# Optimization experiments

Hardware: AMD Instinct MI355X
Metric: run time of the kernel (lower is better)

The kernel has to match this reference:

```python
import jax, jax.numpy as jnp
import numpy as np

N_NODES = 100000
NEG_SLOPE = 0.2


def _gat_conv(x, edge_index, W, att_src, att_dst, bias):
    """Single-head PyG-style GATConv with self-loops.
    x: [N, F_in], edge_index: [2, E] (row 0 = src j, row 1 = dst i).
    """
    N = x.shape[0]
    h = x @ W  # [N, F_out]
    # add self-loops
    loop = jnp.arange(N, dtype=edge_index.dtype)
    src = jnp.concatenate([edge_index[0], loop])
    dst = jnp.concatenate([edge_index[1], loop])
    # per-node attention terms, gathered per edge
    a_s = h @ att_src  # [N]
    a_d = h @ att_dst  # [N]
    e = jax.nn.leaky_relu(a_s[src] + a_d[dst], NEG_SLOPE)  # [E+N]
    # segment softmax over incoming edges of each destination
    m = jax.ops.segment_max(e, dst, num_segments=N)  # [N]
    m = jnp.where(jnp.isfinite(m), m, 0.0)
    p = jnp.exp(e - m[dst])
    denom = jax.ops.segment_sum(p, dst, num_segments=N)  # [N], >0 due to self-loops
    alpha = p / denom[dst]  # [E+N]
    # scatter-aggregate weighted source features
    out = jax.ops.segment_sum(h[src] * alpha[:, None], dst, num_segments=N)
    return out + bias


def setup_inputs() -> dict:
    key = jax.random.key(0)
    ks = jax.random.split(key, 12)
    F_in, H, C = 128, 64, 40
    x = jax.random.normal(ks[0], (N_NODES, F_in), dtype=jnp.float32)
    edge_index = jax.random.randint(ks[1], (2, 1600000), 0, N_NODES, dtype=jnp.int64)
    s1 = 1.0 / np.sqrt(F_in)
    s2 = 1.0 / np.sqrt(H)
    return {
        "x": x,
        "edge_index": edge_index,
        "W1": jax.random.uniform(ks[2], (F_in, H), jnp.float32, -s1, s1),
        "att_src1": jax.random.uniform(ks[3], (H,), jnp.float32, -s2, s2),
        "att_dst1": jax.random.uniform(ks[4], (H,), jnp.float32, -s2, s2),
        "b1": jnp.zeros((H,), jnp.float32),
        "W2": jax.random.uniform(ks[5], (H, C), jnp.float32, -s2, s2),
        "att_src2": jax.random.uniform(ks[6], (C,), jnp.float32, -1.0 / np.sqrt(C), 1.0 / np.sqrt(C)),
        "att_dst2": jax.random.uniform(ks[7], (C,), jnp.float32, -1.0 / np.sqrt(C), 1.0 / np.sqrt(C)),
        "b2": jnp.zeros((C,), jnp.float32),
    }


def reference(x, edge_index, W1, att_src1, att_dst1, b1, W2, att_src2, att_dst2, b2):
    h = _gat_conv(x, edge_index, W1, att_src1, att_dst1, b1)
    h = jax.nn.relu(h)
    # dropout is identity in eval mode
    out = _gat_conv(h, edge_index, W2, att_src2, att_dst2, b2)
    return out
```

## Files before the change

### kernel.cpp

```cpp
#include <hip/hip_runtime.h>
#include <math.h>


#define NEG_SLOPE 0.2f
#define BIN_SHIFT 8
#define BIN_NODES 256
#define MAXBINS   512
#define CAPB      4864
#define K1_CHUNK  4096
#define MAXDEG    128
#define AGG_STRIDE 132
#define XS1 136

typedef _Float16 h4_t __attribute__((ext_vector_type(4)));
typedef _Float16 h8_t __attribute__((ext_vector_type(8)));
typedef float    f16x_t __attribute__((ext_vector_type(16)));

__device__ __forceinline__ float lrelu(float v) {
    return v > 0.f ? v : NEG_SLOPE * v;
}

__global__ __launch_bounds__(256) void prep_kernel(
    const float* __restrict__ W1, const float* __restrict__ W2,
    const float* __restrict__ as1, const float* __restrict__ ad1,
    const float* __restrict__ as2, const float* __restrict__ ad2,
    _Float16* __restrict__ w1f, _Float16* __restrict__ w2f,
    float* __restrict__ u1, float* __restrict__ v1,
    int* __restrict__ bin_cursor)
{
    const int tid = threadIdx.x;
    if (blockIdx.x == 0) {
        for (int j = tid; j < MAXBINS; j += 256) bin_cursor[j] = 0;
        for (int i = tid; i < 8192; i += 256) {
            int j = i & 7, l = (i >> 3) & 63, q = i >> 9;
            int kc = q & 7, ch = q >> 3;
            int n = ch * 32 + (l & 31);
            int k = (l >> 5) * 8 + kc * 16 + j;
            w1f[i] = (_Float16)W1[k * 64 + n];
        }
        if (tid < 128) {
            float su = 0.f, sv = 0.f;
            for (int n = 0; n < 64; ++n) {
                float w = W1[tid * 64 + n];
                su += w * as1[n];
                sv += w * ad1[n];
            }
            u1[tid] = su; v1[tid] = sv;
        }
    } else {
        __shared__ float u2l[64], v2l[64];
        if (tid < 64) {
            float su = 0.f, sv = 0.f;
            for (int n = 0; n < 40; ++n) {
                float w = W2[tid * 40 + n];
                su += w * as2[n];
                sv += w * ad2[n];
            }
            u2l[tid] = su; v2l[tid] = sv;
        }
        __syncthreads();
        for (int i = tid; i < 4096; i += 256) {
            int j = i & 7, l = (i >> 3) & 63, q = i >> 9;
            int kc = q & 3, ch = q >> 2;
            int n = ch * 32 + (l & 31);
            int k = (l >> 5) * 8 + kc * 16 + j;
            _Float16 o = (_Float16)0.f;
            if (n < 40)       o = (_Float16)W2[k * 40 + n];
            else if (n == 40) o = (_Float16)u2l[k];
            else if (n == 41) o = (_Float16)v2l[k];
            w2f[i] = o;
        }
    }
}

__global__ __launch_bounds__(256) void gemm1_bin_kernel(
    const float* __restrict__ x, const _Float16* __restrict__ w1f,
    const float* __restrict__ u1, const float* __restrict__ v1,
    _Float16* __restrict__ h, float* __restrict__ as_, float* __restrict__ ad_,
    int N, int gb,
    const int* __restrict__ src, const int* __restrict__ dst, int E, int nbins,
    int* __restrict__ bin_cursor, int* __restrict__ binned)
{
    __shared__ __align__(16) char smem[18432];
    const int tid = threadIdx.x;

    if (blockIdx.x < gb) {
        _Float16* Xs = (_Float16*)smem;
        float*    Us = (float*)(smem + 17408);
        float*    Vs = (float*)(smem + 17920);
        const int lane = tid & 63;
        const int w = tid >> 6;
        const int rh = w >> 1, ch = w & 1;
        const long rowbase = (long)blockIdx.x * 64;

        {
            const float4* X4 = (const float4*)x;
            const long gmax = (long)N * 32;
#pragma unroll
            for (int i = 0; i < 8; ++i) {
                int f = tid + i * 256;
                int row = f >> 5, c4 = f & 31;
                long gi = (rowbase + row) * 32 + c4;
                float4 v = (gi < gmax) ? X4[gi] : make_float4(0.f, 0.f, 0.f, 0.f);
                h4_t hv;
                hv.x = (_Float16)v.x; hv.y = (_Float16)v.y;
                hv.z = (_Float16)v.z; hv.w = (_Float16)v.w;
                *(h4_t*)&Xs[row * XS1 + c4 * 4] = hv;
            }
        }
        if (tid < 128) Us[tid] = u1[tid];
        else { int t = tid - 128; Vs[t] = v1[t]; }
        __syncthreads();

        {
            const int arow = tid >> 2, apart = tid & 3;
            const _Float16* xr = &Xs[arow * XS1 + apart * 32];
            float ps = 0.f, pd = 0.f;
#pragma unroll
            for (int k = 0; k < 32; k += 4) {
                h4_t xv = *(const h4_t*)(xr + k);
                float4 uu = *(const float4*)&Us[apart * 32 + k];
                float4 vv = *(const float4*)&Vs[apart * 32 + k];
                float x0 = (float)xv.x, x1 = (float)xv.y, x2 = (float)xv.z, x3 = (float)xv.w;
                ps += x0 * uu.x + x1 * uu.y + x2 * uu.z + x3 * uu.w;
                pd += x0 * vv.x + x1 * vv.y + x2 * vv.z + x3 * vv.w;
            }
            ps += __shfl_xor(ps, 1); ps += __shfl_xor(ps, 2);
            pd += __shfl_xor(pd, 1); pd += __shfl_xor(pd, 2);
            if (apart == 0 && rowbase + arow < N) {
                as_[rowbase + arow] = ps;
                ad_[rowbase + arow] = pd;
            }
        }

        const int m = lane & 31, khalf = lane >> 5;
        const _Float16* ax = &Xs[(rh * 32 + m) * XS1 + khalf * 8];
        const h8_t* bF = (const h8_t*)w1f + ch * 8 * 64 + lane;

        f16x_t acc = {};
#pragma unroll
        for (int kc = 0; kc < 8; ++kc) {
            h8_t a = *(const h8_t*)(ax + kc * 16);
            h8_t b = bF[kc * 64];
            acc = __builtin_amdgcn_mfma_f32_32x32x16_f16(a, b, acc, 0, 0, 0);
        }

        const int col = ch * 32 + m;
#pragma unroll
        for (int r = 0; r < 16; ++r) {
            int rowl = (r & 3) + 8 * (r >> 2) + 4 * khalf;
            long grow = rowbase + rh * 32 + rowl;
            if (grow < N) h[grow * 64 + col] = (_Float16)acc[r];
        }
    } else {
        int* hist = (int*)smem;
        int* base = (int*)(smem + 2048);
        int* lcur = (int*)(smem + 4096);
        const int e0 = (blockIdx.x - gb) * K1_CHUNK;

        int sreg[16], dreg[16];
#pragma unroll
        for (int k = 0; k < 16; ++k) {
            int e = e0 + tid + k * 256;
            bool ok = e < E;
            dreg[k] = ok ? dst[e] : -1;
            sreg[k] = ok ? src[e] : 0;
        }

        for (int j = tid; j < nbins; j += 256) hist[j] = 0;
        __syncthreads();
#pragma unroll
        for (int k = 0; k < 16; ++k)
            if (dreg[k] >= 0) atomicAdd(&hist[dreg[k] >> BIN_SHIFT], 1);
        __syncthreads();
        for (int j = tid; j < nbins; j += 256) {
            int c = hist[j];
            base[j] = (c > 0) ? atomicAdd(&bin_cursor[j], c) : 0;
            lcur[j] = 0;
        }
        __syncthreads();
#pragma unroll
        for (int k = 0; k < 16; ++k) {
            if (dreg[k] >= 0) {
                int b = dreg[k] >> BIN_SHIFT;
                int o = atomicAdd(&lcur[b], 1);
                int pos = base[b] + o;
                if (pos < CAPB)
                    binned[b * CAPB + pos] =
                        (sreg[k] << BIN_SHIFT) | (dreg[k] & (BIN_NODES - 1));
            }
        }
    }
}

__global__ __launch_bounds__(512) void fine_kernel(
    const int* __restrict__ bin_cursor, const int* __restrict__ binned,
    int* __restrict__ csr, int* __restrict__ rowptr, int N, int nbins)
{
    __shared__ int a[MAXBINS];
    __shared__ int nh[BIN_NODES];
    __shared__ int cur[BIN_NODES];
    __shared__ int lbuf[CAPB];
    __shared__ int sb[2];
    const int b = blockIdx.x;
    const int tid = threadIdx.x;

    int v = (tid < nbins) ? min(bin_cursor[tid], CAPB) : 0;
    a[tid] = v;
    __syncthreads();
#pragma unroll
    for (int ofs = 1; ofs < MAXBINS; ofs <<= 1) {
        int t = (tid >= ofs) ? a[tid - ofs] : 0;
        __syncthreads();
        a[tid] += t;
        __syncthreads();
    }
    if (tid == 0) {
        sb[0] = (b > 0) ? a[b - 1] : 0;
        sb[1] = a[nbins - 1];
    }

    const int cnt = min(bin_cursor[b], CAPB);
    const int nn = min(BIN_NODES, N - b * BIN_NODES);
    const int* __restrict__ brec = binned + (long)b * CAPB;

    if (tid < BIN_NODES) nh[tid] = 0;
    __syncthreads();

    for (int k = tid; k < cnt; k += 512) {
        atomicAdd(&nh[brec[k] & (BIN_NODES - 1)], 1);
    }
    __syncthreads();

    int hv = (tid < BIN_NODES) ? nh[tid] : 0;
#pragma unroll
    for (int ofs = 1; ofs < BIN_NODES; ofs <<= 1) {
        int t = (tid >= ofs && tid < BIN_NODES) ? nh[tid - ofs] : 0;
        __syncthreads();
        if (tid < BIN_NODES) nh[tid] += t;
        __syncthreads();
    }
    const int binbase = sb[0];
    if (tid < BIN_NODES) {
        int excl = nh[tid] - hv;
        if (tid < nn) rowptr[b * BIN_NODES + tid] = binbase + excl;
        cur[tid] = excl;
    }
    if (b == nbins - 1 && tid == 0) rowptr[N] = sb[1];
    __syncthreads();

    for (int k = tid; k < cnt; k += 512) {
        int rec = brec[k];
        int pos = atomicAdd(&cur[rec & (BIN_NODES - 1)], 1);
        lbuf[pos] = rec >> BIN_SHIFT;
    }
    __syncthreads();
    for (int t = tid; t < cnt; t += 512) {
        csr[binbase + t] = lbuf[t];
    }
}

#define XS2 72
__global__ __launch_bounds__(256) void gemm2_kernel(
    const _Float16* __restrict__ hin, const _Float16* __restrict__ w2f,
    _Float16* __restrict__ h2, float* __restrict__ as_, float* __restrict__ ad_,
    int N)
{
    __shared__ __align__(16) _Float16 Xs[64 * XS2];
    const int tid = threadIdx.x;
    const int lane = tid & 63;
    const int w = tid >> 6;
    const int rh = w >> 1, ch = w & 1;
    const long rowbase = (long)blockIdx.x * 64;

    {
        const h8_t* X8 = (const h8_t*)hin;
        const long gmax = (long)N * 8;
#pragma unroll
        for (int i = 0; i < 2; ++i) {
            int f = tid + i * 256;
            int row = f >> 3, c = f & 7;
            long gi = (rowbase + row) * 8 + c;
            h8_t v = {};
            if (gi < gmax) v = X8[gi];
#pragma unroll
            for (int j = 0; j < 8; ++j) v[j] = (v[j] > (_Float16)0.f) ? v[j] : (_Float16)0.f;
            *(h8_t*)&Xs[row * XS2 + c * 8] = v;
        }
    }
    __syncthreads();

    const int m = lane & 31, khalf = lane >> 5;
    const _Float16* ax = &Xs[(rh * 32 + m) * XS2 + khalf * 8];
    const h8_t* bF = (const h8_t*)w2f + ch * 4 * 64 + lane;

    f16x_t acc = {};
#pragma unroll
    for (int kc = 0; kc < 4; ++kc) {
        h8_t a = *(const h8_t*)(ax + kc * 16);
        h8_t b = bF[kc * 64];
        acc = __builtin_amdgcn_mfma_f32_32x32x16_f16(a, b, acc, 0, 0, 0);
    }

    const int col = ch * 32 + m;
#pragma unroll
    for (int r = 0; r < 16; ++r) {
        int rowl = (r & 3) + 8 * (r >> 2) + 4 * khalf;
        long grow = rowbase + rh * 32 + rowl;
        float v = acc[r];
        if (grow < N) {
            if (col < 40)       h2[grow * 40 + col] = (_Float16)v;
            else if (col == 40) as_[grow] = v;
            else if (col == 41) ad_[grow] = v;
        }
    }
}

template<int F, typename OT>
__global__ __launch_bounds__(256) void aggregate_kernel(
    const _Float16* __restrict__ h, const float* __restrict__ as_,
    const float* __restrict__ ad_, const int* __restrict__ rowptr,
    const int* __restrict__ csr, const float* __restrict__ bias,
    OT* __restrict__ out, int N)
{
    __shared__ __align__(16) int   Ss[16 * AGG_STRIDE];
    __shared__ __align__(16) float Ps[16 * AGG_STRIDE];
    const int tid = threadIdx.x;
    const int dl  = tid >> 4;
    const int sub = tid & 15;
    const int i = blockIdx.x * 16 + dl;
    const bool alive = (i < N);

    int r0 = 0, deg = 0;
    if (alive) {
        r0 = rowptr[i];
        deg = rowptr[i + 1] - r0;
        if (deg > MAXDEG) deg = MAXDEG;
    }
    const float adi    = alive ? ad_[i] : 0.f;
    const float e_self = alive ? lrelu(as_[i] + adi) : 0.f;

    int*   __restrict__ sp = &Ss[dl * AGG_STRIDE];
    float* __restrict__ pp = &Ps[dl * AGG_STRIDE];

    float psum = 0.f;
    for (int c = sub; c < deg; c += 16) {
        int s = csr[r0 + c];
        float p = __expf(lrelu(as_[s] + adi));
        sp[c] = s;
        pp[c] = p;
        psum += p;
    }
#pragma unroll
    for (int off = 1; off < 16; off <<= 1) psum += __shfl_xor(psum, off);
    const float p_self = __expf(e_self);
    const float inv = 1.f / (psum + p_self);

    const bool act = (sub * 4 < F);
    const int  col = act ? sub * 4 : 0;
    float4 acc = make_float4(0.f, 0.f, 0.f, 0.f);

    int k = 0;
    for (; k + 8 <= deg; k += 8) {
        int4   s0 = *(const int4*)&sp[k];
        int4   s1 = *(const int4*)&sp[k + 4];
        float4 p0 = *(const float4*)&pp[k];
        float4 p1 = *(const float4*)&pp[k + 4];
        if (act) {
            h4_t hA = *(const h4_t*)&h[(long)s0.x * F + col];
            h4_t hB = *(const h4_t*)&h[(long)s0.y * F + col];
            h4_t hC = *(const h4_t*)&h[(long)s0.z * F + col];
            h4_t hD = *(const h4_t*)&h[(long)s0.w * F + col];
            h4_t hE = *(const h4_t*)&h[(long)s1.x * F + col];
            h4_t hF = *(const h4_t*)&h[(long)s1.y * F + col];
            h4_t hG = *(const h4_t*)&h[(long)s1.z * F + col];
            h4_t hH = *(const h4_t*)&h[(long)s1.w * F + col];
            acc.x += (float)hA.x * p0.x + (float)hB.x * p0.y + (float)hC.x * p0.z + (float)hD.x * p0.w
                   + (float)hE.x * p1.x + (float)hF.x * p1.y + (float)hG.x * p1.z + (float)hH.x * p1.w;
            acc.y += (float)hA.y * p0.x + (float)hB.y * p0.y + (float)hC.y * p0.z + (float)hD.y * p0.w
                   + (float)hE.y * p1.x + (float)hF.y * p1.y + (float)hG.y * p1.z + (float)hH.y * p1.w;
            acc.z += (float)hA.z * p0.x + (float)hB.z * p0.y + (float)hC.z * p0.z + (float)hD.z * p0.w
                   + (float)hE.z * p1.x + (float)hF.z * p1.y + (float)hG.z * p1.z + (float)hH.z * p1.w;
            acc.w += (float)hA.w * p0.x + (float)hB.w * p0.y + (float)hC.w * p0.z + (float)hD.w * p0.w
                   + (float)hE.w * p1.x + (float)hF.w * p1.y + (float)hG.w * p1.z + (float)hH.w * p1.w;
        }
    }
    for (; k + 4 <= deg; k += 4) {
        int4   s0 = *(const int4*)&sp[k];
        float4 p0 = *(const float4*)&pp[k];
        if (act) {
            h4_t hA = *(const h4_t*)&h[(long)s0.x * F + col];
            h4_t hB = *(const h4_t*)&h[(long)s0.y * F + col];
            h4_t hC = *(const h4_t*)&h[(long)s0.z * F + col];
            h4_t hD = *(const h4_t*)&h[(long)s0.w * F + col];
            acc.x += (float)hA.x * p0.x + (float)hB.x * p0.y + (float)hC.x * p0.z + (float)hD.x * p0.w;
            acc.y += (float)hA.y * p0.x + (float)hB.y * p0.y + (float)hC.y * p0.z + (float)hD.y * p0.w;
            acc.z += (float)hA.z * p0.x + (float)hB.z * p0.y + (float)hC.z * p0.z + (float)hD.z * p0.w;
            acc.w += (float)hA.w * p0.x + (float)hB.w * p0.y + (float)hC.w * p0.z + (float)hD.w * p0.w;
        }
    }
    for (; k < deg; ++k) {
        int   s = sp[k];
        float p = pp[k];
        if (act) {
            h4_t hv = *(const h4_t*)&h[(long)s * F + col];
            acc.x += (float)hv.x * p; acc.y += (float)hv.y * p;
            acc.z += (float)hv.z * p; acc.w += (float)hv.w * p;
        }
    }

    if (alive && act) {
        h4_t hv = *(const h4_t*)&h[(long)i * F + col];
        float4 bv = *(const float4*)&bias[col];
        float ox = (acc.x + (float)hv.x * p_self) * inv + bv.x;
        float oy = (acc.y + (float)hv.y * p_self) * inv + bv.y;
        float oz = (acc.z + (float)hv.z * p_self) * inv + bv.z;
        float ow = (acc.w + (float)hv.w * p_self) * inv + bv.w;
        if constexpr (sizeof(OT) == 4) {
            float4 o = make_float4(ox, oy, oz, ow);
            *(float4*)&out[(long)i * F + col] = o;
        } else {
            h4_t o;
            o.x = (_Float16)ox; o.y = (_Float16)oy;
            o.z = (_Float16)oz; o.w = (_Float16)ow;
            *(h4_t*)&out[(long)i * F + col] = o;
        }
    }
}

extern "C" void kernel_launch(void* const* d_in, const int* in_sizes, int n_in,
                              void* d_out, int out_size, void* d_ws, size_t ws_size,
                              hipStream_t stream) {
    const float* x    = (const float*)d_in[0];
    const int*   ei   = (const int*)d_in[1];
    const float* W1   = (const float*)d_in[2];
    const float* at_s1= (const float*)d_in[3];
    const float* at_d1= (const float*)d_in[4];
    const float* b1   = (const float*)d_in[5];
    const float* W2   = (const float*)d_in[6];
    const float* at_s2= (const float*)d_in[7];
    const float* at_d2= (const float*)d_in[8];
    const float* b2   = (const float*)d_in[9];
    float* out = (float*)d_out;

    const int N = in_sizes[0] / 128;
    const int E = in_sizes[1] / 2;
    const int nbins = (N + BIN_NODES - 1) >> BIN_SHIFT;

    char* p = (char*)d_ws;
    auto carve = [&](size_t bytes) -> void* {
        void* r = (void*)p;
        p += (bytes + 255) & ~(size_t)255;
        return r;
    };
    int*       bin_cursor = (int*)      carve((size_t)MAXBINS * 4);
    int*       binned     = (int*)      carve((size_t)nbins * CAPB * 4);
    int*       csr        = (int*)      carve((size_t)E * 4);
    int*       rowptr     = (int*)      carve((size_t)(N + 1) * 4);
    _Float16*  w1f        = (_Float16*) carve((size_t)8192 * 2);
    _Float16*  w2f        = (_Float16*) carve((size_t)4096 * 2);
    float*     u1         = (float*)    carve((size_t)128 * 4);
    float*     v1         = (float*)    carve((size_t)128 * 4);
    _Float16*  h1         = (_Float16*) carve((size_t)N * 64 * 2);
    _Float16*  agg1h      = (_Float16*) carve((size_t)N * 64 * 2);
    _Float16*  h2         = (_Float16*) carve((size_t)N * 40 * 2);
    float*     asn        = (float*)    carve((size_t)N * 4);
    float*     adn        = (float*)    carve((size_t)N * 4);

    prep_kernel<<<2, 256, 0, stream>>>(W1, W2, at_s1, at_d1, at_s2, at_d2,
                                       w1f, w2f, u1, v1, bin_cursor);

    const int gb = (N + 63) / 64;
    const int bb = (E + K1_CHUNK - 1) / K1_CHUNK;
    gemm1_bin_kernel<<<gb + bb, 256, 0, stream>>>(
        x, w1f, u1, v1, h1, asn, adn, N, gb,
        ei, ei + E, E, nbins, bin_cursor, binned);

    fine_kernel<<<nbins, 512, 0, stream>>>(bin_cursor, binned, csr, rowptr, N, nbins);

    aggregate_kernel<64, _Float16><<<(N + 15) / 16, 256, 0, stream>>>(
        h1, asn, adn, rowptr, csr, b1, agg1h, N);

    gemm2_kernel<<<(N + 63) / 64, 256, 0, stream>>>(agg1h, w2f, h2, asn, adn, N);

    aggregate_kernel<40, float><<<(N + 15) / 16, 256, 0, stream>>>(
        h2, asn, adn, rowptr, csr, b2, out, N);
}
```

Measured before the change: 222.9 us.

## Fuse layer-1 aggregation with layer-2 GEMM via per-block MFMA epilogue

Replaces the separate layer-1 aggregate kernel and gemm2 kernel with one kernel. Each 16-node block aggregates its neighbours, applies bias and ReLU, stages the fp16 rows in shared memory, and runs 16x16x32 MFMAs against a repacked W2 (with the attention vectors folded in) to emit h2 and the layer-2 attention scalars. This removes a kernel launch and the write and re-read of the intermediate N x 64 activation. In exchange each block does a small GEMM with only three of its four waves busy, adds a __syncthreads, and uses separate buffers for the layer-2 attention scalars.

Result: faster. 218.3 us (-2.1%).

```diff
diff --git a/kernel.cpp b/kernel.cpp
--- a/kernel.cpp
+++ b/kernel.cpp
@@ -11,10 +11,12 @@
 #define MAXDEG    128
 #define AGG_STRIDE 132
 #define XS1 136
+#define RTS 72
 
 typedef _Float16 h4_t __attribute__((ext_vector_type(4)));
 typedef _Float16 h8_t __attribute__((ext_vector_type(8)));
 typedef float    f16x_t __attribute__((ext_vector_type(16)));
+typedef float    f4_t  __attribute__((ext_vector_type(4)));
 
 __device__ __forceinline__ float lrelu(float v) {
     return v > 0.f ? v : NEG_SLOPE * v;
@@ -24,7 +26,7 @@
     const float* __restrict__ W1, const float* __restrict__ W2,
     const float* __restrict__ as1, const float* __restrict__ ad1,
     const float* __restrict__ as2, const float* __restrict__ ad2,
-    _Float16* __restrict__ w1f, _Float16* __restrict__ w2f,
+    _Float16* __restrict__ w1f, _Float16* __restrict__ w2g,
     float* __restrict__ u1, float* __restrict__ v1,
     int* __restrict__ bin_cursor)
 {
@@ -59,16 +61,16 @@
             u2l[tid] = su; v2l[tid] = sv;
         }
         __syncthreads();
-        for (int i = tid; i < 4096; i += 256) {
+        for (int i = tid; i < 3072; i += 256) {
             int j = i & 7, l = (i >> 3) & 63, q = i >> 9;
-            int kc = q & 3, ch = q >> 2;
-            int n = ch * 32 + (l & 31);
-            int k = (l >> 5) * 8 + kc * 16 + j;
+            int kk = q & 1, cb = q >> 1;
+            int n = cb * 16 + (l & 15);
+            int k = kk * 32 + (l >> 4) * 8 + j;
             _Float16 o = (_Float16)0.f;
             if (n < 40)       o = (_Float16)W2[k * 40 + n];
             else if (n == 40) o = (_Float16)u2l[k];
             else if (n == 41) o = (_Float16)v2l[k];
-            w2f[i] = o;
+            w2g[i] = o;
         }
     }
 }
@@ -260,58 +262,127 @@
     }
 }
 
-#define XS2 72
-__global__ __launch_bounds__(256) void gemm2_kernel(
-    const _Float16* __restrict__ hin, const _Float16* __restrict__ w2f,
-    _Float16* __restrict__ h2, float* __restrict__ as_, float* __restrict__ ad_,
+__global__ __launch_bounds__(256) void agg1_fused_kernel(
+    const _Float16* __restrict__ h, const float* __restrict__ as_,
+    const float* __restrict__ ad_, const int* __restrict__ rowptr,
+    const int* __restrict__ csr, const float* __restrict__ b1,
+    const _Float16* __restrict__ w2g,
+    _Float16* __restrict__ h2, float* __restrict__ as2, float* __restrict__ ad2,
     int N)
 {
-    __shared__ __align__(16) _Float16 Xs[64 * XS2];
+    __shared__ __align__(16) int      Ss[16 * AGG_STRIDE];
+    __shared__ __align__(16) float    Ps[16 * AGG_STRIDE];
+    __shared__ __align__(16) _Float16 Rt[16 * RTS];
     const int tid = threadIdx.x;
-    const int lane = tid & 63;
-    const int w = tid >> 6;
-    const int rh = w >> 1, ch = w & 1;
-    const long rowbase = (long)blockIdx.x * 64;
-
-    {
-        const h8_t* X8 = (const h8_t*)hin;
-        const long gmax = (long)N * 8;
-#pragma unroll
-        for (int i = 0; i < 2; ++i) {
-            int f = tid + i * 256;
-            int row = f >> 3, c = f & 7;
-            long gi = (rowbase + row) * 8 + c;
-            h8_t v = {};
-            if (gi < gmax) v = X8[gi];
-#pragma unroll
-            for (int j = 0; j < 8; ++j) v[j] = (v[j] > (_Float16)0.f) ? v[j] : (_Float16)0.f;
-            *(h8_t*)&Xs[row * XS2 + c * 8] = v;
-        }
-    }
+    const int dl  = tid >> 4;
+    const int sub = tid & 15;
+    const long blockbase = (long)blockIdx.x * 16;
+    const long i = blockbase + dl;
+    const bool alive = (i < N);
+
+    int r0 = 0, deg = 0;
+    if (alive) {
+        r0 = rowptr[i];
+        deg = rowptr[i + 1] - r0;
+        if (deg > MAXDEG) deg = MAXDEG;
+    }
+    const float adi    = alive ? ad_[i] : 0.f;
+    const float e_self = alive ? lrelu(as_[i] + adi) : 0.f;
+
+    int*   __restrict__ sp = &Ss[dl * AGG_STRIDE];
+    float* __restrict__ pp = &Ps[dl * AGG_STRIDE];
+
+    float psum = 0.f;
+    for (int c = sub; c < deg; c += 16) {
+        int s = csr[r0 + c];
+        float p = __expf(lrelu(as_[s] + adi));
+        sp[c] = s;
+        pp[c] = p;
+        psum += p;
+    }
+#pragma unroll
+    for (int off = 1; off < 16; off <<= 1) psum += __shfl_xor(psum, off);
+    const float p_self = __expf(e_self);
+    const float inv = 1.f / (psum + p_self);
+
+    const int col = sub * 4;
+    float4 acc = make_float4(0.f, 0.f, 0.f, 0.f);
+
+    int k = 0;
+    for (; k + 8 <= deg; k += 8) {
+        int4   s0 = *(const int4*)&sp[k];
+        int4   s1 = *(const int4*)&sp[k + 4];
+        float4 p0 = *(const float4*)&pp[k];
+        float4 p1 = *(const float4*)&pp[k + 4];
+        h4_t hA = *(const h4_t*)&h[(long)s0.x * 64 + col];
+        h4_t hB = *(const h4_t*)&h[(long)s0.y * 64 + col];
+        h4_t hC = *(const h4_t*)&h[(long)s0.z * 64 + col];
+        h4_t hD = *(const h4_t*)&h[(long)s0.w * 64 + col];
+        h4_t hE = *(const h4_t*)&h[(long)s1.x * 64 + col];
+        h4_t hF = *(const h4_t*)&h[(long)s1.y * 64 + col];
+        h4_t hG = *(const h4_t*)&h[(long)s1.z * 64 + col];
+        h4_t hH = *(const h4_t*)&h[(long)s1.w * 64 + col];
+        acc.x += (float)hA.x * p0.x + (float)hB.x * p0.y + (float)hC.x * p0.z + (float)hD.x * p0.w
+               + (float)hE.x * p1.x + (float)hF.x * p1.y + (float)hG.x * p1.z + (float)hH.x * p1.w;
+        acc.y += (float)hA.y * p0.x + (float)hB.y * p0.y + (float)hC.y * p0.z + (float)hD.y * p0.w
+               + (float)hE.y * p1.x + (float)hF.y * p1.y + (float)hG.y * p1.z + (float)hH.y * p1.w;
+        acc.z += (float)hA.z * p0.x + (float)hB.z * p0.y + (float)hC.z * p0.z + (float)hD.z * p0.w
+               + (float)hE.z * p1.x + (float)hF.z * p1.y + (float)hG.z * p1.z + (float)hH.z * p1.w;
+        acc.w += (float)hA.w * p0.x + (float)hB.w * p0.y + (float)hC.w * p0.z + (float)hD.w * p0.w
+               + (float)hE.w * p1.x + (float)hF.w * p1.y + (float)hG.w * p1.z + (float)hH.w * p1.w;
+    }
+    for (; k + 4 <= deg; k += 4) {
+        int4   s0 = *(const int4*)&sp[k];
+        float4 p0 = *(const float4*)&pp[k];
+        h4_t hA = *(const h4_t*)&h[(long)s0.x * 64 + col];
+        h4_t hB = *(const h4_t*)&h[(long)s0.y * 64 + col];
+        h4_t hC = *(const h4_t*)&h[(long)s0.z * 64 + col];
+        h4_t hD = *(const h4_t*)&h[(long)s0.w * 64 + col];
+        acc.x += (float)hA.x * p0.x + (float)hB.x * p0.y + (float)hC.x * p0.z + (float)hD.x * p0.w;
+        acc.y += (float)hA.y * p0.x + (float)hB.y * p0.y + (float)hC.y * p0.z + (float)hD.y * p0.w;
+        acc.z += (float)hA.z * p0.x + (float)hB.z * p0.y + (float)hC.z * p0.z + (float)hD.z * p0.w;
+        acc.w += (float)hA.w * p0.x + (float)hB.w * p0.y + (float)hC.w * p0.z + (float)hD.w * p0.w;
+    }
+    for (; k < deg; ++k) {
+        int   s = sp[k];
+        float p = pp[k];
+        h4_t hv = *(const h4_t*)&h[(long)s * 64 + col];
+        acc.x += (float)hv.x * p; acc.y += (float)hv.y * p;
+        acc.z += (float)hv.z * p; acc.w += (float)hv.w * p;
+    }
+
+    h4_t hv = {};
+    if (alive) hv = *(const h4_t*)&h[i * 64 + col];
+    float4 bv = *(const float4*)&b1[col];
+    h4_t rt;
+    rt.x = (_Float16)fmaxf((acc.x + (float)hv.x * p_self) * inv + bv.x, 0.f);
+    rt.y = (_Float16)fmaxf((acc.y + (float)hv.y * p_self) * inv + bv.y, 0.f);
+    rt.z = (_Float16)fmaxf((acc.z + (float)hv.z * p_self) * inv + bv.z, 0.f);
+    rt.w = (_Float16)fmaxf((acc.w + (float)hv.w * p_self) * inv + bv.w, 0.f);
+    *(h4_t*)&Rt[dl * RTS + sub * 4] = rt;
     __syncthreads();
 
-    const int m = lane & 31, khalf = lane >> 5;
-    const _Float16* ax = &Xs[(rh * 32 + m) * XS2 + khalf * 8];
-    const h8_t* bF = (const h8_t*)w2f + ch * 4 * 64 + lane;
-
-    f16x_t acc = {};
-#pragma unroll
-    for (int kc = 0; kc < 4; ++kc) {
-        h8_t a = *(const h8_t*)(ax + kc * 16);
-        h8_t b = bF[kc * 64];
-        acc = __builtin_amdgcn_mfma_f32_32x32x16_f16(a, b, acc, 0, 0, 0);
-    }
-
-    const int col = ch * 32 + m;
-#pragma unroll
-    for (int r = 0; r < 16; ++r) {
-        int rowl = (r & 3) + 8 * (r >> 2) + 4 * khalf;
-        long grow = rowbase + rh * 32 + rowl;
-        float v = acc[r];
-        if (grow < N) {
-            if (col < 40)       h2[grow * 40 + col] = (_Float16)v;
-            else if (col == 40) as_[grow] = v;
-            else if (col == 41) ad_[grow] = v;
+    const int w = tid >> 6, lane = tid & 63;
+    if (w < 3) {
+        const int arow = lane & 15, kq = lane >> 4;
+        f4_t c = {};
+#pragma unroll
+        for (int kk = 0; kk < 2; ++kk) {
+            h8_t a = *(const h8_t*)&Rt[arow * RTS + kk * 32 + kq * 8];
+            h8_t b = ((const h8_t*)w2g)[(w * 2 + kk) * 64 + lane];
+            c = __builtin_amdgcn_mfma_f32_16x16x32_f16(a, b, c, 0, 0, 0);
+        }
+        const int ocol = w * 16 + (lane & 15);
+#pragma unroll
+        for (int r = 0; r < 4; ++r) {
+            int orow = (lane >> 4) * 4 + r;
+            long gi = blockbase + orow;
+            if (gi < N) {
+                float v = c[r];
+                if (ocol < 40)       h2[gi * 40 + ocol] = (_Float16)v;
+                else if (ocol == 40) as2[gi] = v;
+                else if (ocol == 41) ad2[gi] = v;
+            }
         }
     }
 }
@@ -458,17 +529,18 @@
     int*       csr        = (int*)      carve((size_t)E * 4);
     int*       rowptr     = (int*)      carve((size_t)(N + 1) * 4);
     _Float16*  w1f        = (_Float16*) carve((size_t)8192 * 2);
-    _Float16*  w2f        = (_Float16*) carve((size_t)4096 * 2);
+    _Float16*  w2g        = (_Float16*) carve((size_t)3072 * 2);
     float*     u1         = (float*)    carve((size_t)128 * 4);
     float*     v1         = (float*)    carve((size_t)128 * 4);
     _Float16*  h1         = (_Float16*) carve((size_t)N * 64 * 2);
-    _Float16*  agg1h      = (_Float16*) carve((size_t)N * 64 * 2);
     _Float16*  h2         = (_Float16*) carve((size_t)N * 40 * 2);
     float*     asn        = (float*)    carve((size_t)N * 4);
     float*     adn        = (float*)    carve((size_t)N * 4);
+    float*     as2n       = (float*)    carve((size_t)N * 4);
+    float*     ad2n       = (float*)    carve((size_t)N * 4);
 
     prep_kernel<<<2, 256, 0, stream>>>(W1, W2, at_s1, at_d1, at_s2, at_d2,
-                                       w1f, w2f, u1, v1, bin_cursor);
+                                       w1f, w2g, u1, v1, bin_cursor);
 
     const int gb = (N + 63) / 64;
     const int bb = (E + K1_CHUNK - 1) / K1_CHUNK;
@@ -478,11 +550,9 @@
 
     fine_kernel<<<nbins, 512, 0, stream>>>(bin_cursor, binned, csr, rowptr, N, nbins);
 
-    aggregate_kernel<64, _Float16><<<(N + 15) / 16, 256, 0, stream>>>(
-        h1, asn, adn, rowptr, csr, b1, agg1h, N);
-
-    gemm2_kernel<<<(N + 63) / 64, 256, 0, stream>>>(agg1h, w2f, h2, asn, adn, N);
+    agg1_fused_kernel<<<(N + 15) / 16, 256, 0, stream>>>(
+        h1, asn, adn, rowptr, csr, b1, w2g, h2, as2n, ad2n, N);
 
     aggregate_kernel<40, float><<<(N + 15) / 16, 256, 0, stream>>>(
-        h2, asn, adn, rowptr, csr, b2, out, N);
-}
+        h2, as2n, ad2n, rowptr, csr, b2, out, N);
+}
```
